# Kernel tuning notes

Hardware: AMD Instinct MI355X
Metric: run time of the kernel (lower is better)

The kernel has to match this reference:

```python
import jax, jax.numpy as jnp
import numpy as np

B = 4096
DIM = 2048
B1 = 25   # root children (level-2 inner nodes)
B2 = 40   # leaves per level-2 node
NUM_CLASSES = B1 * B2  # 1000


def setup_inputs() -> dict:
    key = jax.random.key(0)
    k1, k2, k3, k4 = jax.random.split(key, 4)
    x = jax.random.normal(k1, (B, DIM), dtype=jnp.float32)
    labels = jax.random.randint(k2, (B,), 0, NUM_CLASSES, dtype=jnp.int64)
    # per-node Linear(dim, num_child + 1); column 0 = 'not in subtree'
    W_root = jax.random.normal(k3, (DIM, B1 + 1), dtype=jnp.float32) * 0.02
    b_root = jnp.zeros((B1 + 1,), dtype=jnp.float32)
    W_lvl2 = jax.random.normal(k4, (B1, DIM, B2 + 1), dtype=jnp.float32) * 0.02
    b_lvl2 = jnp.zeros((B1, B2 + 1), dtype=jnp.float32)
    return {"x": x, "labels": labels, "W_root": W_root, "b_root": b_root,
            "W_lvl2": W_lvl2, "b_lvl2": b_lvl2}


def reference(x, labels, W_root, b_root, W_lvl2, b_lvl2):
    b = x.shape[0]
    b1 = W_lvl2.shape[0]
    b2 = W_lvl2.shape[2] - 1

    # layer 1: root classifier (root.path_prob == 1.0)
    root_logits = x @ W_root + b_root                       # [B, b1+1]
    root_lp = jax.nn.log_softmax(root_logits, axis=-1)
    root_prob = jnp.exp(root_lp)

    # layer 2: all level-2 node classifiers as one grouped GEMM
    lvl2_logits = jnp.einsum('bd,ndk->bnk', x, W_lvl2) + b_lvl2  # [B, b1, b2+1]
    lvl2_lp = jax.nn.log_softmax(lvl2_logits, axis=-1)
    lvl2_prob = jnp.exp(lvl2_lp)

    # leaf path_prob = P(child under node n) * P(node n under root);
    # leaves tile out columns contiguously (label2id of complete tree)
    out = (lvl2_prob[:, :, 1:] * root_prob[:, 1:, None]).reshape(b, b1 * b2)

    # penalty: CE at each inner node divided by its layer l
    j = labels // b2                                        # level-2 parent index
    i = labels % b2                                         # leaf index within parent
    ce_root = -jnp.take_along_axis(root_lp, (j + 1)[:, None], axis=1).mean()
    # sub-label for node n: i+1 if label's parent is n, else 0
    sub_lab = jnp.where(j[:, None] == jnp.arange(b1)[None, :], (i + 1)[:, None], 0)
    gathered = jnp.take_along_axis(lvl2_lp, sub_lab[:, :, None], axis=2)[..., 0]  # [B, b1]
    penalty = ce_root + (-gathered).mean(axis=0).sum() / 2.0

    return out, penalty
```

## Files before the change

### kernel.cpp

```cpp
#include <hip/hip_runtime.h>
#include <stdint.h>

#define TB 256

typedef __bf16 bf16x8 __attribute__((ext_vector_type(8)));
typedef float f32x4 __attribute__((ext_vector_type(4)));

#define AS1 __attribute__((address_space(1)))
#define AS3 __attribute__((address_space(3)))
#define GLOAD16(gp, lp) __builtin_amdgcn_global_load_lds( \
    (const AS1 unsigned int*)(gp), (AS3 unsigned int*)(lp), 16, 0, 0)

__device__ __forceinline__ unsigned short f2bf(float f) {
  uint32_t u = __builtin_bit_cast(uint32_t, f);
  u += 0x7fffu + ((u >> 16) & 1u);
  return (unsigned short)(u >> 16);
}

__global__ __launch_bounds__(TB) void k_xcvt(const float* __restrict__ x,
                                             unsigned short* __restrict__ xbf) {
  int idx = blockIdx.x * TB + threadIdx.x;
  const float4* xin = reinterpret_cast<const float4*>(x);
  float4 a = xin[idx * 2], b = xin[idx * 2 + 1];
  uint32_t p0 = f2bf(a.x) | ((uint32_t)f2bf(a.y) << 16);
  uint32_t p1 = f2bf(a.z) | ((uint32_t)f2bf(a.w) << 16);
  uint32_t p2 = f2bf(b.x) | ((uint32_t)f2bf(b.y) << 16);
  uint32_t p3 = f2bf(b.z) | ((uint32_t)f2bf(b.w) << 16);
  reinterpret_cast<uint4*>(xbf)[idx] = make_uint4(p0, p1, p2, p3);
}

__global__ __launch_bounds__(TB) void k_wt(const float* __restrict__ wl,
                                           const float* __restrict__ wr,
                                           unsigned short* __restrict__ wlt,
                                           unsigned short* __restrict__ wrt) {
  __shared__ float ld_f[2624];
  int bid = blockIdx.x;
  int t = threadIdx.x;
  if (bid < 800) {
    int n = bid / 32, dt = bid % 32, d0 = dt * 64;
    const float* src = wl + ((size_t)n * 2048 + d0) * 41;
    for (int i = 0; i < 11; i++) { int lin = t + TB * i; if (lin < 2624) ld_f[lin] = src[lin]; }
    __syncthreads();
    unsigned short* dst = wlt + (size_t)n * 48 * 2048 + d0;
    for (int i = 0; i < 12; i++) {
      int lin = t + TB * i;
      int wc = lin >> 6, d = lin & 63;
      float v = (wc < 41) ? ld_f[d * 41 + wc] : 0.f;
      dst[(size_t)wc * 2048 + d] = f2bf(v);
    }
  } else {
    int dt = bid - 800, d0 = dt * 64;
    const float* src = wr + (size_t)d0 * 26;
    for (int i = 0; i < 7; i++) { int lin = t + TB * i; if (lin < 1664) ld_f[lin] = src[lin]; }
    __syncthreads();
    unsigned short* dst = wrt + d0;
    for (int i = 0; i < 8; i++) {
      int lin = t + TB * i;
      int wc = lin >> 6, d = lin & 63;
      float v = (wc < 26) ? ld_f[d * 26 + wc] : 0.f;
      dst[(size_t)wc * 2048 + d] = f2bf(v);
    }
  }
}

__global__ __launch_bounds__(TB) void k_labfix(const int* __restrict__ lin_,
                                               int* __restrict__ lout,
                                               float* __restrict__ pengl) {
  __shared__ int orred;
  int t = threadIdx.x;
  if (t == 0) { orred = 0; pengl[0] = 0.f; }
  __syncthreads();
  int acc = 0;
  for (int i = t; i < 2048; i += TB) acc |= lin_[2 * i + 1];
  atomicOr(&orred, acc);
  __syncthreads();
  bool i64 = (orred == 0);
  for (int i = t; i < 4096; i += TB) lout[i] = i64 ? lin_[2 * i] : lin_[i];
}

__device__ __forceinline__ void stage_x(const unsigned short* xg, unsigned char* lbuf,
                                        int kk, int tid, int wavebase) {
#pragma unroll
  for (int i = 0; i < 4; i++) {
    int c = i * 256 + tid;
    int row = c >> 3, s = c & 7;
    const unsigned short* gp = xg + (size_t)row * 2048 + kk + ((s ^ (row & 7)) << 3);
    GLOAD16(gp, lbuf + (size_t)(i * 256 + wavebase) * 16);
  }
}

__global__ __launch_bounds__(TB) void k_rootg(const unsigned short* __restrict__ xbf,
                                              const unsigned short* __restrict__ wrt,
                                              float* __restrict__ wslog) {
  __shared__ __align__(16) unsigned char lds[2][20480];
  int bid = blockIdx.x;
  int rt = bid >> 3, ks8 = bid & 7;
  int r0 = rt * 128, kbase = ks8 * 256;
  int tid = threadIdx.x, lane = tid & 63, wave = tid >> 6;
  int wavebase = wave * 64;
  int lq = lane >> 4, lr = lane & 15;
  f32x4 acc[2][2] = {};
  const unsigned short* xg = xbf + (size_t)r0 * 2048;

#define STAGE_R(bufi, kk)                                                        \
  do {                                                                           \
    stage_x(xg, lds[bufi], (kk), tid, wavebase);                                 \
    int wc = tid >> 3, s = tid & 7;                                              \
    const unsigned short* gp = wrt + (size_t)wc * 2048 + (kk) + ((s ^ (wc & 7)) << 3); \
    GLOAD16(gp, lds[bufi] + 16384 + (size_t)wavebase * 16);                      \
  } while (0)

  STAGE_R(0, kbase);
  __syncthreads();
  int cur = 0;
#pragma unroll
  for (int t = 0; t < 4; t++) {
    if (t < 3) STAGE_R(cur ^ 1, kbase + (t + 1) * 64);
    unsigned char* base = &lds[cur][0];
#pragma unroll
    for (int ks = 0; ks < 2; ks++) {
      bf16x8 af[2], bx[2];
#pragma unroll
      for (int mt = 0; mt < 2; mt++) {
        int wc = mt * 16 + lr;
        af[mt] = *reinterpret_cast<const bf16x8*>(base + 16384 + wc * 128 + ((((ks << 2) | lq) ^ (wc & 7)) << 4));
      }
#pragma unroll
      for (int nt = 0; nt < 2; nt++) {
        int row = wave * 32 + nt * 16 + lr;
        bx[nt] = *reinterpret_cast<const bf16x8*>(base + row * 128 + ((((ks << 2) | lq) ^ (row & 7)) << 4));
      }
#pragma unroll
      for (int mt = 0; mt < 2; mt++)
#pragma unroll
        for (int nt = 0; nt < 2; nt++)
          acc[mt][nt] = __builtin_amdgcn_mfma_f32_16x16x32_bf16(af[mt], bx[nt], acc[mt][nt], 0, 0, 0);
    }
    __syncthreads();
    cur ^= 1;
  }
#pragma unroll
  for (int nt = 0; nt < 2; nt++) {
    int b = r0 + wave * 32 + nt * 16 + lr;
#pragma unroll
    for (int mt = 0; mt < 2; mt++)
#pragma unroll
      for (int r = 0; r < 4; r++) {
        int wc = mt * 16 + lq * 4 + r;
        if (wc < 26) atomicAdd(&wslog[(size_t)b * 32 + wc], acc[mt][nt][r]);
      }
  }
}

__global__ __launch_bounds__(TB) void k_rootsm(const float* __restrict__ wslog,
                                               const float* __restrict__ br,
                                               const int* __restrict__ labels,
                                               float* __restrict__ rootp,
                                               float* __restrict__ pengl) {
  int b = blockIdx.x * TB + threadIdx.x;
  float lgs[26];
  float m = -1e30f;
#pragma unroll
  for (int c = 0; c < 26; c++) { lgs[c] = wslog[(size_t)b * 32 + c] + br[c]; m = fmaxf(m, lgs[c]); }
  float s = 0.f;
#pragma unroll
  for (int c = 0; c < 26; c++) s += expf(lgs[c] - m);
  float ls = logf(s);
#pragma unroll
  for (int c = 0; c < 26; c++) rootp[(size_t)b * 32 + c] = expf(lgs[c] - m - ls);
  int lab = labels[b];
  int j = lab / 40;
  float pen = 0.f;
#pragma unroll
  for (int c = 0; c < 26; c++) if (c == j + 1) pen = -(lgs[c] - m - ls);
  for (int off = 32; off; off >>= 1) pen += __shfl_down(pen, off);
  __shared__ float red[4];
  int lane = threadIdx.x & 63, wave = threadIdx.x >> 6;
  if (lane == 0) red[wave] = pen;
  __syncthreads();
  if (threadIdx.x == 0) atomicAdd(pengl, (red[0] + red[1] + red[2] + red[3]) * (1.f / 4096.f));
}

__global__ __launch_bounds__(TB) void k_lvl2(const unsigned short* __restrict__ xbf,
                                             const unsigned short* __restrict__ wlt,
                                             const float* __restrict__ bl,
                                             const int* __restrict__ labels,
                                             const float* __restrict__ rootp,
                                             float* __restrict__ out,
                                             float* __restrict__ pengl) {
  __shared__ __align__(16) unsigned char lds[2][22528];
  int bid = blockIdx.x;
  int swz = (bid & 7) * 100 + (bid >> 3);
  int rt = swz / 25, n = swz % 25;
  int r0 = rt * 128;
  int tid = threadIdx.x, lane = tid & 63, wave = tid >> 6;
  int wavebase = wave * 64;
  int lq = lane >> 4, lr = lane & 15;
  f32x4 acc[3][2] = {};
  const unsigned short* xg = xbf + (size_t)r0 * 2048;
  const unsigned short* wg = wlt + (size_t)n * 48 * 2048;

#define STAGE_L(bufi, kk)                                                        \
  do {                                                                           \
    stage_x(xg, lds[bufi], (kk), tid, wavebase);                                 \
    {                                                                            \
      int wc = tid >> 3, s = tid & 7;                                            \
      const unsigned short* gp = wg + (size_t)wc * 2048 + (kk) + ((s ^ (wc & 7)) << 3); \
      GLOAD16(gp, lds[bufi] + 16384 + (size_t)wavebase * 16);                    \
    }                                                                            \
    if (tid < 128) {                                                             \
      int c = 256 + tid;                                                         \
      int wc = c >> 3, s = c & 7;                                                \
      const unsigned short* gp = wg + (size_t)wc * 2048 + (kk) + ((s ^ (wc & 7)) << 3); \
      GLOAD16(gp, lds[bufi] + 16384 + (size_t)(256 + wavebase) * 16);            \
    }                                                                            \
  } while (0)

  STAGE_L(0, 0);
  __syncthreads();
  int cur = 0;
  for (int kk = 0; kk < 2048; kk += 64) {
    if (kk + 64 < 2048) STAGE_L(cur ^ 1, kk + 64);
    unsigned char* base = &lds[cur][0];
#pragma unroll
    for (int ks = 0; ks < 2; ks++) {
      bf16x8 af[3], bx[2];
#pragma unroll
      for (int mt = 0; mt < 3; mt++) {
        int wc = mt * 16 + lr;
        af[mt] = *reinterpret_cast<const bf16x8*>(base + 16384 + wc * 128 + ((((ks << 2) | lq) ^ (wc & 7)) << 4));
      }
#pragma unroll
      for (int nt = 0; nt < 2; nt++) {
        int row = wave * 32 + nt * 16 + lr;
        bx[nt] = *reinterpret_cast<const bf16x8*>(base + row * 128 + ((((ks << 2) | lq) ^ (row & 7)) << 4));
      }
#pragma unroll
      for (int mt = 0; mt < 3; mt++)
#pragma unroll
        for (int nt = 0; nt < 2; nt++)
          acc[mt][nt] = __builtin_amdgcn_mfma_f32_16x16x32_bf16(af[mt], bx[nt], acc[mt][nt], 0, 0, 0);
    }
    __syncthreads();
    cur ^= 1;
  }

  float bb[3][4];
#pragma unroll
  for (int mt = 0; mt < 3; mt++)
#pragma unroll
    for (int r = 0; r < 4; r++) {
      int wc = mt * 16 + lq * 4 + r;
      bb[mt][r] = (wc < 41) ? bl[n * 41 + wc] : -1e30f;
    }
  float pen = 0.f;
#pragma unroll
  for (int nt = 0; nt < 2; nt++) {
    int b = r0 + wave * 32 + nt * 16 + lr;
    float lg[3][4];
    float m = -1e30f;
#pragma unroll
    for (int mt = 0; mt < 3; mt++)
#pragma unroll
      for (int r = 0; r < 4; r++) {
        float v = acc[mt][nt][r] + bb[mt][r];
        lg[mt][r] = v;
        m = fmaxf(m, v);
      }
    m = fmaxf(m, __shfl_xor(m, 16));
    m = fmaxf(m, __shfl_xor(m, 32));
    float s = 0.f;
#pragma unroll
    for (int mt = 0; mt < 3; mt++)
#pragma unroll
      for (int r = 0; r < 4; r++) s += expf(lg[mt][r] - m);
    s += __shfl_xor(s, 16);
    s += __shfl_xor(s, 32);
    float ls = logf(s);
    float rp = rootp[(size_t)b * 32 + (n + 1)];
    int lab = labels[b];
    int j = lab / 40;
    int sub = (j == n) ? (lab - j * 40 + 1) : 0;
#pragma unroll
    for (int mt = 0; mt < 3; mt++)
#pragma unroll
      for (int r = 0; r < 4; r++) {
        int wc = mt * 16 + lq * 4 + r;
        float lp = lg[mt][r] - m - ls;
        if (wc >= 1 && wc < 41) out[(size_t)b * 1000 + n * 40 + wc - 1] = expf(lp) * rp;
        if (wc == sub) pen -= lp;
      }
  }
  for (int off = 32; off; off >>= 1) pen += __shfl_down(pen, off);
  float* red = (float*)&lds[0][0];
  if (lane == 0) red[wave] = pen;
  __syncthreads();
  if (tid == 0) atomicAdd(pengl, (red[0] + red[1] + red[2] + red[3]) * (1.f / 8192.f));
}

extern "C" void kernel_launch(void* const* d_in, const int* in_sizes, int n_in,
                              void* d_out, int out_size, void* d_ws, size_t ws_size,
                              hipStream_t stream) {
  const float* x = (const float*)d_in[0];
  const int* labels_raw = (const int*)d_in[1];
  const float* wroot = (const float*)d_in[2];
  const float* broot = (const float*)d_in[3];
  const float* wlvl2 = (const float*)d_in[4];
  const float* blvl2 = (const float*)d_in[5];
  float* out = (float*)d_out;
  float* pengl = out + 4096000;

  char* ws = (char*)d_ws;
  unsigned short* xbf = (unsigned short*)ws;
  unsigned short* wlt = (unsigned short*)(ws + 16777216);
  unsigned short* wrt = (unsigned short*)(ws + 16777216 + 4915200);
  float* wslog = (float*)(ws + 16777216 + 4915200 + 131072);
  float* rootp = (float*)(ws + 16777216 + 4915200 + 131072 + 524288);
  int* lab32 = (int*)(ws + 16777216 + 4915200 + 131072 + 524288 + 524288);

  hipMemsetAsync(wslog, 0, 4096 * 32 * 4, stream);
  k_labfix<<<1, TB, 0, stream>>>(labels_raw, lab32, pengl);
  k_xcvt<<<4096, TB, 0, stream>>>(x, xbf);
  k_wt<<<832, TB, 0, stream>>>(wlvl2, wroot, wlt, wrt);
  k_rootg<<<256, TB, 0, stream>>>(xbf, wrt, wslog);
  k_rootsm<<<16, TB, 0, stream>>>(wslog, broot, lab32, rootp, pengl);
  k_lvl2<<<800, TB, 0, stream>>>(xbf, wlt, blvl2, lab32, rootp, out, pengl);
}
```

Measured before the change: 173.1 us.

## Merge prep kernels, fuse root GEMM with softmax, triple-buffer GEMM pipelines

Folds the x conversion, weight transposes and label fixup into one prep launch. Replaces the split-K root GEMM, its atomic accumulation, the memset and the separate softmax kernel with a single full-K root kernel that computes the softmax and penalty in registers. Both GEMM kernels move from double-buffered LDS with __syncthreads to a three-stage ring using explicit partial vmcnt waits, so global-to-LDS loads overlap more compute. The level-2 weights are padded to 64 rows so every thread issues uniform loads; the price is more LDS per block and only 64 blocks for the root GEMM.

```diff
diff --git a/kernel.cpp b/kernel.cpp
--- a/kernel.cpp
+++ b/kernel.cpp
@@ -17,168 +17,198 @@
   return (unsigned short)(u >> 16);
 }
 
-__global__ __launch_bounds__(TB) void k_xcvt(const float* __restrict__ x,
-                                             unsigned short* __restrict__ xbf) {
-  int idx = blockIdx.x * TB + threadIdx.x;
-  const float4* xin = reinterpret_cast<const float4*>(x);
-  float4 a = xin[idx * 2], b = xin[idx * 2 + 1];
-  uint32_t p0 = f2bf(a.x) | ((uint32_t)f2bf(a.y) << 16);
-  uint32_t p1 = f2bf(a.z) | ((uint32_t)f2bf(a.w) << 16);
-  uint32_t p2 = f2bf(b.x) | ((uint32_t)f2bf(b.y) << 16);
-  uint32_t p3 = f2bf(b.z) | ((uint32_t)f2bf(b.w) << 16);
-  reinterpret_cast<uint4*>(xbf)[idx] = make_uint4(p0, p1, p2, p3);
-}
-
-__global__ __launch_bounds__(TB) void k_wt(const float* __restrict__ wl,
-                                           const float* __restrict__ wr,
-                                           unsigned short* __restrict__ wlt,
-                                           unsigned short* __restrict__ wrt) {
-  __shared__ float ld_f[2624];
-  int bid = blockIdx.x;
-  int t = threadIdx.x;
-  if (bid < 800) {
-    int n = bid / 32, dt = bid % 32, d0 = dt * 64;
-    const float* src = wl + ((size_t)n * 2048 + d0) * 41;
-    for (int i = 0; i < 11; i++) { int lin = t + TB * i; if (lin < 2624) ld_f[lin] = src[lin]; }
+__device__ __forceinline__ void waitbar6() {
+  __builtin_amdgcn_sched_barrier(0);
+  asm volatile("s_waitcnt vmcnt(6) lgkmcnt(0)" ::: "memory");
+  __builtin_amdgcn_s_barrier();
+  __builtin_amdgcn_sched_barrier(0);
+}
+__device__ __forceinline__ void waitbar3() {
+  __builtin_amdgcn_sched_barrier(0);
+  asm volatile("s_waitcnt vmcnt(3) lgkmcnt(0)" ::: "memory");
+  __builtin_amdgcn_s_barrier();
+  __builtin_amdgcn_sched_barrier(0);
+}
+__device__ __forceinline__ void waitbar0() {
+  __builtin_amdgcn_sched_barrier(0);
+  asm volatile("s_waitcnt vmcnt(0) lgkmcnt(0)" ::: "memory");
+  __builtin_amdgcn_s_barrier();
+  __builtin_amdgcn_sched_barrier(0);
+}
+
+__global__ __launch_bounds__(TB) void k_prep(const float* __restrict__ x,
+                                             const float* __restrict__ wl,
+                                             const float* __restrict__ wr,
+                                             const int* __restrict__ labraw,
+                                             unsigned short* __restrict__ xbf,
+                                             unsigned short* __restrict__ wlt,
+                                             unsigned short* __restrict__ wrt,
+                                             int* __restrict__ lab32,
+                                             float* __restrict__ pengl) {
+  int bid = blockIdx.x, t = threadIdx.x;
+  if (bid < 4096) {
+    int idx = bid * TB + t;
+    const float4* xin = reinterpret_cast<const float4*>(x);
+    float4 a = xin[idx * 2], b = xin[idx * 2 + 1];
+    uint32_t p0 = f2bf(a.x) | ((uint32_t)f2bf(a.y) << 16);
+    uint32_t p1 = f2bf(a.z) | ((uint32_t)f2bf(a.w) << 16);
+    uint32_t p2 = f2bf(b.x) | ((uint32_t)f2bf(b.y) << 16);
+    uint32_t p3 = f2bf(b.z) | ((uint32_t)f2bf(b.w) << 16);
+    reinterpret_cast<uint4*>(xbf)[idx] = make_uint4(p0, p1, p2, p3);
+  } else if (bid < 4928) {
+    __shared__ float ld_f[2624];
+    int b2 = bid - 4096;
+    if (b2 < 800) {
+      int n = b2 / 32, dt = b2 % 32, d0 = dt * 64;
+      const float* src = wl + ((size_t)n * 2048 + d0) * 41;
+      for (int i = 0; i < 11; i++) { int lin = t + TB * i; if (lin < 2624) ld_f[lin] = src[lin]; }
+      __syncthreads();
+      unsigned short* dst = wlt + (size_t)n * 64 * 2048 + d0;
+      for (int i = 0; i < 12; i++) {
+        int lin = t + TB * i;
+        int wc = lin >> 6, d = lin & 63;
+        float v = (wc < 41) ? ld_f[d * 41 + wc] : 0.f;
+        dst[(size_t)wc * 2048 + d] = f2bf(v);
+      }
+    } else {
+      int dt = b2 - 800, d0 = dt * 64;
+      const float* src = wr + (size_t)d0 * 26;
+      for (int i = 0; i < 7; i++) { int lin = t + TB * i; if (lin < 1664) ld_f[lin] = src[lin]; }
+      __syncthreads();
+      unsigned short* dst = wrt + d0;
+      for (int i = 0; i < 8; i++) {
+        int lin = t + TB * i;
+        int wc = lin >> 6, d = lin & 63;
+        float v = (wc < 26) ? ld_f[d * 26 + wc] : 0.f;
+        dst[(size_t)wc * 2048 + d] = f2bf(v);
+      }
+    }
+  } else {
+    __shared__ int orred;
+    if (t == 0) { orred = 0; pengl[0] = 0.f; }
     __syncthreads();
-    unsigned short* dst = wlt + (size_t)n * 48 * 2048 + d0;
-    for (int i = 0; i < 12; i++) {
-      int lin = t + TB * i;
-      int wc = lin >> 6, d = lin & 63;
-      float v = (wc < 41) ? ld_f[d * 41 + wc] : 0.f;
-      dst[(size_t)wc * 2048 + d] = f2bf(v);
-    }
-  } else {
-    int dt = bid - 800, d0 = dt * 64;
-    const float* src = wr + (size_t)d0 * 26;
-    for (int i = 0; i < 7; i++) { int lin = t + TB * i; if (lin < 1664) ld_f[lin] = src[lin]; }
+    int acc = 0;
+    for (int i = t; i < 2048; i += TB) acc |= labraw[2 * i + 1];
+    atomicOr(&orred, acc);
     __syncthreads();
-    unsigned short* dst = wrt + d0;
-    for (int i = 0; i < 8; i++) {
-      int lin = t + TB * i;
-      int wc = lin >> 6, d = lin & 63;
-      float v = (wc < 26) ? ld_f[d * 26 + wc] : 0.f;
-      dst[(size_t)wc * 2048 + d] = f2bf(v);
-    }
+    bool i64 = (orred == 0);
+    for (int i = t; i < 4096; i += TB) lab32[i] = i64 ? labraw[2 * i] : labraw[i];
   }
 }
 
-__global__ __launch_bounds__(TB) void k_labfix(const int* __restrict__ lin_,
-                                               int* __restrict__ lout,
-                                               float* __restrict__ pengl) {
-  __shared__ int orred;
-  int t = threadIdx.x;
-  if (t == 0) { orred = 0; pengl[0] = 0.f; }
-  __syncthreads();
-  int acc = 0;
-  for (int i = t; i < 2048; i += TB) acc |= lin_[2 * i + 1];
-  atomicOr(&orred, acc);
-  __syncthreads();
-  bool i64 = (orred == 0);
-  for (int i = t; i < 4096; i += TB) lout[i] = i64 ? lin_[2 * i] : lin_[i];
-}
-
-__device__ __forceinline__ void stage_x(const unsigned short* xg, unsigned char* lbuf,
-                                        int kk, int tid, int wavebase) {
-#pragma unroll
-  for (int i = 0; i < 4; i++) {
-    int c = i * 256 + tid;
-    int row = c >> 3, s = c & 7;
-    const unsigned short* gp = xg + (size_t)row * 2048 + kk + ((s ^ (row & 7)) << 3);
-    GLOAD16(gp, lbuf + (size_t)(i * 256 + wavebase) * 16);
-  }
-}
-
-__global__ __launch_bounds__(TB) void k_rootg(const unsigned short* __restrict__ xbf,
-                                              const unsigned short* __restrict__ wrt,
-                                              float* __restrict__ wslog) {
-  __shared__ __align__(16) unsigned char lds[2][20480];
-  int bid = blockIdx.x;
-  int rt = bid >> 3, ks8 = bid & 7;
-  int r0 = rt * 128, kbase = ks8 * 256;
+__global__ __launch_bounds__(TB) void k_root(const unsigned short* __restrict__ xbf,
+                                             const unsigned short* __restrict__ wrt,
+                                             const float* __restrict__ br,
+                                             const int* __restrict__ labels,
+                                             float* __restrict__ rootp,
+                                             float* __restrict__ pengl) {
+  __shared__ __align__(16) unsigned char lds3[3][12288];
+  int r0 = blockIdx.x * 64;
   int tid = threadIdx.x, lane = tid & 63, wave = tid >> 6;
   int wavebase = wave * 64;
   int lq = lane >> 4, lr = lane & 15;
-  f32x4 acc[2][2] = {};
   const unsigned short* xg = xbf + (size_t)r0 * 2048;
-
-#define STAGE_R(bufi, kk)                                                        \
-  do {                                                                           \
-    stage_x(xg, lds[bufi], (kk), tid, wavebase);                                 \
-    int wc = tid >> 3, s = tid & 7;                                              \
-    const unsigned short* gp = wrt + (size_t)wc * 2048 + (kk) + ((s ^ (wc & 7)) << 3); \
-    GLOAD16(gp, lds[bufi] + 16384 + (size_t)wavebase * 16);                      \
+  f32x4 acc[2] = {};
+
+#define STAGE_RT(lb, kk)                                                              \
+  do {                                                                                \
+    _Pragma("unroll")                                                                 \
+    for (int i = 0; i < 2; i++) {                                                     \
+      int c = i * 256 + tid;                                                          \
+      int row = c >> 3, s = c & 7;                                                    \
+      const unsigned short* gp = xg + (size_t)row * 2048 + (kk) + ((s ^ (row & 7)) << 3); \
+      GLOAD16(gp, (lb) + (size_t)(i * 256 + wavebase) * 16);                          \
+    }                                                                                 \
+    {                                                                                 \
+      int wc = tid >> 3, s = tid & 7;                                                 \
+      const unsigned short* gp = wrt + (size_t)wc * 2048 + (kk) + ((s ^ (wc & 7)) << 3); \
+      GLOAD16(gp, (lb) + 8192 + (size_t)wavebase * 16);                               \
+    }                                                                                 \
   } while (0)
 
-  STAGE_R(0, kbase);
-  __syncthreads();
+#define COMPUTE_RT(base)                                                              \
+  do {                                                                                \
+    _Pragma("unroll")                                                                 \
+    for (int ks = 0; ks < 2; ks++) {                                                  \
+      bf16x8 af[2], bx;                                                               \
+      _Pragma("unroll")                                                               \
+      for (int mt = 0; mt < 2; mt++) {                                                \
+        int wc = mt * 16 + lr;                                                        \
+        af[mt] = *reinterpret_cast<const bf16x8*>((base) + 8192 + wc * 128 + ((((ks << 2) | lq) ^ (wc & 7)) << 4)); \
+      }                                                                               \
+      {                                                                               \
+        int row = wavebase / 4 + lr;                                \
+        bx = *reinterpret_cast<const bf16x8*>((base) + row * 128 + ((((ks << 2) | lq) ^ (row & 7)) << 4)); \
+      }                                                                               \
+      _Pragma("unroll")                                                               \
+      for (int mt = 0; mt < 2; mt++)                                                  \
+        acc[mt] = __builtin_amdgcn_mfma_f32_16x16x32_bf16(af[mt], bx, acc[mt], 0, 0, 0); \
+    }                                                                                 \
+  } while (0)
+
+  STAGE_RT(&lds3[0][0], 0);
+  STAGE_RT(&lds3[1][0], 64);
+  waitbar3();
   int cur = 0;
-#pragma unroll
-  for (int t = 0; t < 4; t++) {
-    if (t < 3) STAGE_R(cur ^ 1, kbase + (t + 1) * 64);
-    unsigned char* base = &lds[cur][0];
-#pragma unroll
-    for (int ks = 0; ks < 2; ks++) {
-      bf16x8 af[2], bx[2];
-#pragma unroll
-      for (int mt = 0; mt < 2; mt++) {
-        int wc = mt * 16 + lr;
-        af[mt] = *reinterpret_cast<const bf16x8*>(base + 16384 + wc * 128 + ((((ks << 2) | lq) ^ (wc & 7)) << 4));
-      }
-#pragma unroll
-      for (int nt = 0; nt < 2; nt++) {
-        int row = wave * 32 + nt * 16 + lr;
-        bx[nt] = *reinterpret_cast<const bf16x8*>(base + row * 128 + ((((ks << 2) | lq) ^ (row & 7)) << 4));
-      }
-#pragma unroll
-      for (int mt = 0; mt < 2; mt++)
-#pragma unroll
-        for (int nt = 0; nt < 2; nt++)
-          acc[mt][nt] = __builtin_amdgcn_mfma_f32_16x16x32_bf16(af[mt], bx[nt], acc[mt][nt], 0, 0, 0);
-    }
-    __syncthreads();
-    cur ^= 1;
+#pragma unroll 3
+  for (int t = 0; t < 30; ++t) {
+    int nx = cur + 2; if (nx >= 3) nx -= 3;
+    STAGE_RT(&lds3[nx][0], (t + 2) * 64);
+    COMPUTE_RT(&lds3[cur][0]);
+    waitbar3();
+    ++cur; if (cur == 3) cur = 0;
   }
-#pragma unroll
-  for (int nt = 0; nt < 2; nt++) {
-    int b = r0 + wave * 32 + nt * 16 + lr;
-#pragma unroll
-    for (int mt = 0; mt < 2; mt++)
-#pragma unroll
-      for (int r = 0; r < 4; r++) {
-        int wc = mt * 16 + lq * 4 + r;
-        if (wc < 26) atomicAdd(&wslog[(size_t)b * 32 + wc], acc[mt][nt][r]);
-      }
-  }
-}
-
-__global__ __launch_bounds__(TB) void k_rootsm(const float* __restrict__ wslog,
-                                               const float* __restrict__ br,
-                                               const int* __restrict__ labels,
-                                               float* __restrict__ rootp,
-                                               float* __restrict__ pengl) {
-  int b = blockIdx.x * TB + threadIdx.x;
-  float lgs[26];
+  COMPUTE_RT(&lds3[cur][0]);
+  waitbar0();
+  ++cur; if (cur == 3) cur = 0;
+  COMPUTE_RT(&lds3[cur][0]);
+
+  float bb[2][4];
+#pragma unroll
+  for (int mt = 0; mt < 2; mt++)
+#pragma unroll
+    for (int r = 0; r < 4; r++) {
+      int wc = mt * 16 + lq * 4 + r;
+      bb[mt][r] = (wc < 26) ? br[wc] : -1e30f;
+    }
+  int b = r0 + wave * 16 + lr;
+  float lg[2][4];
   float m = -1e30f;
 #pragma unroll
-  for (int c = 0; c < 26; c++) { lgs[c] = wslog[(size_t)b * 32 + c] + br[c]; m = fmaxf(m, lgs[c]); }
+  for (int mt = 0; mt < 2; mt++)
+#pragma unroll
+    for (int r = 0; r < 4; r++) {
+      float v = acc[mt][r] + bb[mt][r];
+      lg[mt][r] = v;
+      m = fmaxf(m, v);
+    }
+  m = fmaxf(m, __shfl_xor(m, 16));
+  m = fmaxf(m, __shfl_xor(m, 32));
   float s = 0.f;
 #pragma unroll
-  for (int c = 0; c < 26; c++) s += expf(lgs[c] - m);
+  for (int mt = 0; mt < 2; mt++)
+#pragma unroll
+    for (int r = 0; r < 4; r++) s += expf(lg[mt][r] - m);
+  s += __shfl_xor(s, 16);
+  s += __shfl_xor(s, 32);
   float ls = logf(s);
-#pragma unroll
-  for (int c = 0; c < 26; c++) rootp[(size_t)b * 32 + c] = expf(lgs[c] - m - ls);
   int lab = labels[b];
   int j = lab / 40;
   float pen = 0.f;
 #pragma unroll
-  for (int c = 0; c < 26; c++) if (c == j + 1) pen = -(lgs[c] - m - ls);
+  for (int mt = 0; mt < 2; mt++)
+#pragma unroll
+    for (int r = 0; r < 4; r++) {
+      int wc = mt * 16 + lq * 4 + r;
+      float lp = lg[mt][r] - m - ls;
+      if (wc < 26) rootp[(size_t)b * 32 + wc] = expf(lp);
+      if (wc == j + 1) pen -= lp;
+    }
   for (int off = 32; off; off >>= 1) pen += __shfl_down(pen, off);
-  __shared__ float red[4];
-  int lane = threadIdx.x & 63, wave = threadIdx.x >> 6;
+  float* red = (float*)&lds3[0][0];
   if (lane == 0) red[wave] = pen;
   __syncthreads();
-  if (threadIdx.x == 0) atomicAdd(pengl, (red[0] + red[1] + red[2] + red[3]) * (1.f / 4096.f));
+  if (tid == 0) atomicAdd(pengl, (red[0] + red[1] + red[2] + red[3]) * (1.f / 4096.f));
 }
 
 __global__ __launch_bounds__(TB) void k_lvl2(const unsigned short* __restrict__ xbf,
@@ -188,7 +218,7 @@
                                              const float* __restrict__ rootp,
                                              float* __restrict__ out,
                                              float* __restrict__ pengl) {
-  __shared__ __align__(16) unsigned char lds[2][22528];
+  __shared__ __align__(16) unsigned char lds3[3][24576];
   int bid = blockIdx.x;
   int swz = (bid & 7) * 100 + (bid >> 3);
   int rt = swz / 25, n = swz % 25;
@@ -198,52 +228,65 @@
   int lq = lane >> 4, lr = lane & 15;
   f32x4 acc[3][2] = {};
   const unsigned short* xg = xbf + (size_t)r0 * 2048;
-  const unsigned short* wg = wlt + (size_t)n * 48 * 2048;
-
-#define STAGE_L(bufi, kk)                                                        \
-  do {                                                                           \
-    stage_x(xg, lds[bufi], (kk), tid, wavebase);                                 \
-    {                                                                            \
-      int wc = tid >> 3, s = tid & 7;                                            \
+  const unsigned short* wg = wlt + (size_t)n * 64 * 2048;
+
+#define STAGE_L2(lb, kk)                                                              \
+  do {                                                                                \
+    _Pragma("unroll")                                                                 \
+    for (int i = 0; i < 4; i++) {                                                     \
+      int c = i * 256 + tid;                                                          \
+      int row = c >> 3, s = c & 7;                                                    \
+      const unsigned short* gp = xg + (size_t)row * 2048 + (kk) + ((s ^ (row & 7)) << 3); \
+      GLOAD16(gp, (lb) + (size_t)(i * 256 + wavebase) * 16);                          \
+    }                                                                                 \
+    _Pragma("unroll")                                                                 \
+    for (int i = 0; i < 2; i++) {                                                     \
+      int c = i * 256 + tid;                                                          \
+      int wc = c >> 3, s = c & 7;                                                     \
       const unsigned short* gp = wg + (size_t)wc * 2048 + (kk) + ((s ^ (wc & 7)) << 3); \
-      GLOAD16(gp, lds[bufi] + 16384 + (size_t)wavebase * 16);                    \
-    }                                                                            \
-    if (tid < 128) {                                                             \
-      int c = 256 + tid;                                                         \
-      int wc = c >> 3, s = c & 7;                                                \
-      const unsigned short* gp = wg + (size_t)wc * 2048 + (kk) + ((s ^ (wc & 7)) << 3); \
-      GLOAD16(gp, lds[bufi] + 16384 + (size_t)(256 + wavebase) * 16);            \
-    }                                                                            \
+      GLOAD16(gp, (lb) + 16384 + (size_t)(i * 256 + wavebase) * 16);                  \
+    }                                                                                 \
   } while (0)
 
-  STAGE_L(0, 0);
-  __syncthreads();
+#define COMPUTE_L2(base)                                                              \
+  do {                                                                                \
+    _Pragma("unroll")                                                                 \
+    for (int ks = 0; ks < 2; ks++) {                                                  \
+      bf16x8 af[3], bx[2];                                                            \
+      _Pragma("unroll")                                                               \
+      for (int mt = 0; mt < 3; mt++) {                                                \
+        int wc = mt * 16 + lr;                                                        \
+        af[mt] = *reinterpret_cast<const bf16x8*>((base) + 16384 + wc * 128 + ((((ks << 2) | lq) ^ (wc & 7)) << 4)); \
+      }                                                                               \
+      _Pragma("unroll")                                                               \
+      for (int nt = 0; nt < 2; nt++) {                                                \
+        int row = wave * 32 + nt * 16 + lr;                                           \
+        bx[nt] = *reinterpret_cast<const bf16x8*>((base) + row * 128 + ((((ks << 2) | lq) ^ (row & 7)) << 4)); \
+      }                                                                               \
+      _Pragma("unroll")                                                               \
+      for (int mt = 0; mt < 3; mt++)                                                  \
+        _Pragma("unroll")                                                             \
+        for (int nt = 0; nt < 2; nt++)                                                \
+          acc[mt][nt] = __builtin_amdgcn_mfma_f32_16x16x32_bf16(af[mt], bx[nt], acc[mt][nt], 0, 0, 0); \
+    }                                                                                 \
+  } while (0)
+
+  STAGE_L2(&lds3[0][0], 0);
+  STAGE_L2(&lds3[1][0], 64);
+  waitbar6();
   int cur = 0;
-  for (int kk = 0; kk < 2048; kk += 64) {
-    if (kk + 64 < 2048) STAGE_L(cur ^ 1, kk + 64);
-    unsigned char* base = &lds[cur][0];
-#pragma unroll
-    for (int ks = 0; ks < 2; ks++) {
-      bf16x8 af[3], bx[2];
-#pragma unroll
-      for (int mt = 0; mt < 3; mt++) {
-        int wc = mt * 16 + lr;
-        af[mt] = *reinterpret_cast<const bf16x8*>(base + 16384 + wc * 128 + ((((ks << 2) | lq) ^ (wc & 7)) << 4));
-      }
-#pragma unroll
-      for (int nt = 0; nt < 2; nt++) {
-        int row = wave * 32 + nt * 16 + lr;
-        bx[nt] = *reinterpret_cast<const bf16x8*>(base + row * 128 + ((((ks << 2) | lq) ^ (row & 7)) << 4));
-      }
-#pragma unroll
-      for (int mt = 0; mt < 3; mt++)
-#pragma unroll
-        for (int nt = 0; nt < 2; nt++)
-          acc[mt][nt] = __builtin_amdgcn_mfma_f32_16x16x32_bf16(af[mt], bx[nt], acc[mt][nt], 0, 0, 0);
-    }
-    __syncthreads();
-    cur ^= 1;
+#pragma unroll 3
+  for (int t = 0; t < 30; ++t) {
+    int nx = cur + 2; if (nx >= 3) nx -= 3;
+    STAGE_L2(&lds3[nx][0], (t + 2) * 64);
+    COMPUTE_L2(&lds3[cur][0]);
+    waitbar6();
+    ++cur; if (cur == 3) cur = 0;
   }
+  COMPUTE_L2(&lds3[cur][0]);
+  waitbar0();
+  ++cur; if (cur == 3) cur = 0;
+  COMPUTE_L2(&lds3[cur][0]);
 
   float bb[3][4];
 #pragma unroll
@@ -292,7 +335,7 @@
       }
   }
   for (int off = 32; off; off >>= 1) pen += __shfl_down(pen, off);
-  float* red = (float*)&lds[0][0];
+  float* red = (float*)&lds3[0][0];
   if (lane == 0) red[wave] = pen;
   __syncthreads();
   if (tid == 0) atomicAdd(pengl, (red[0] + red[1] + red[2] + red[3]) * (1.f / 8192.f));
@@ -313,16 +356,11 @@
   char* ws = (char*)d_ws;
   unsigned short* xbf = (unsigned short*)ws;
   unsigned short* wlt = (unsigned short*)(ws + 16777216);
-  unsigned short* wrt = (unsigned short*)(ws + 16777216 + 4915200);
-  float* wslog = (float*)(ws + 16777216 + 4915200 + 131072);
-  float* rootp = (float*)(ws + 16777216 + 4915200 + 131072 + 524288);
-  int* lab32 = (int*)(ws + 16777216 + 4915200 + 131072 + 524288 + 524288);
-
-  hipMemsetAsync(wslog, 0, 4096 * 32 * 4, stream);
-  k_labfix<<<1, TB, 0, stream>>>(labels_raw, lab32, pengl);
-  k_xcvt<<<4096, TB, 0, stream>>>(x, xbf);
-  k_wt<<<832, TB, 0, stream>>>(wlvl2, wroot, wlt, wrt);
-  k_rootg<<<256, TB, 0, stream>>>(xbf, wrt, wslog);
-  k_rootsm<<<16, TB, 0, stream>>>(wslog, broot, lab32, rootp, pengl);
+  unsigned short* wrt = (unsigned short*)(ws + 16777216 + 6553600);
+  float* rootp = (float*)(ws + 16777216 + 6553600 + 131072);
+  int* lab32 = (int*)(ws + 16777216 + 6553600 + 131072 + 524288);
+
+  k_prep<<<4929, TB, 0, stream>>>(x, wlvl2, wroot, labels_raw, xbf, wlt, wrt, lab32, pengl);
+  k_root<<<64, TB, 0, stream>>>(xbf, wrt, broot, lab32, rootp, pengl);
   k_lvl2<<<800, TB, 0, stream>>>(xbf, wlt, blvl2, lab32, rootp, out, pengl);
 }
```

Measured after the change: 152.8 us. -11.7%, faster.
